# Optimization experiments

Measured on AMD Instinct MI355X. Metric: run time of the kernel, lower is better.

The kernel has to match this reference:

```python
import jax, jax.numpy as jnp
import numpy as np

B, L = 1024, 1024
NCAT, NNUM = 20, 10
CAT_BUCKETS, SEQ_VOCAB = 100000, 50000
E, A, H, QH = 32, 128, 256, 256
TOPK = 30


def _init(key, shape, scale=0.02):
    return scale * jax.random.normal(key, shape, dtype=jnp.float32)


def setup_inputs() -> dict:
    key = jax.random.key(0)
    ks = jax.random.split(key, 24)
    z = lambda *s: jnp.zeros(s, dtype=jnp.float32)
    return {
        "cats": jax.random.randint(ks[0], (B, NCAT), 0, CAT_BUCKETS + 1),
        "nums": jax.random.normal(ks[1], (B, NNUM), dtype=jnp.float32),
        "seqs": jax.random.randint(ks[2], (B, L), 0, SEQ_VOCAB + 1),
        "tgt_ids": jax.random.randint(ks[3], (B,), 0, CAT_BUCKETS + 1),
        "cat_emb": _init(ks[4], (CAT_BUCKETS + 1, E)),
        "seq_emb": _init(ks[5], (SEQ_VOCAB + 1, E)),
        "Wnum": _init(ks[6], (NNUM, E)), "bnum": z(E),
        "Wq": _init(ks[7], (E, A)), "Wk": _init(ks[8], (E, A)), "Wv": _init(ks[9], (E, A)),
        "Wo": _init(ks[10], (A, E)), "bo": z(E),
        "Wpool": _init(ks[11], (NCAT * E, E)), "bpool": z(E),
        "Wmlp": _init(ks[12], (4 * E, H)), "bmlp": z(H),
        "q1_W1": _init(ks[13], (H, QH)), "q1_b1": z(QH),
        "q1_W2": _init(ks[14], (H, QH)), "q1_b2": z(QH),
        "q1_Wp": _init(ks[15], (QH, H)), "q1_bp": z(H),
        "q2_W1": _init(ks[16], (H, QH)), "q2_b1": z(QH),
        "q2_W2": _init(ks[17], (H, QH)), "q2_b2": z(QH),
        "q2_Wp": _init(ks[18], (QH, H)), "q2_bp": z(H),
        "Wout": _init(ks[19], (H, 1)), "bout": z(1),
    }


def _qnn(x, W1, b1, W2, b2, Wp, bp):
    # Quadratic neural block (QIN-style): Hadamard product of two linear maps,
    # projected back with a residual connection. Dropout is identity in eval.
    quad = (x @ W1 + b1) * (x @ W2 + b2)
    return x + quad @ Wp + bp


def reference(cats, nums, seqs, tgt_ids, cat_emb, seq_emb, Wnum, bnum, Wq, Wk, Wv,
              Wo, bo, Wpool, bpool, Wmlp, bmlp,
              q1_W1, q1_b1, q1_W2, q1_b2, q1_Wp, q1_bp,
              q2_W1, q2_b1, q2_W2, q2_b2, q2_Wp, q2_bp, Wout, bout):
    cat_e = cat_emb[cats]                                   # [B, NCAT, E]
    cat_pool = cat_e.reshape(cat_e.shape[0], -1) @ Wpool + bpool   # [B, E]
    num_e = nums @ Wnum + bnum                              # [B, E]
    tgt_e = cat_emb[tgt_ids]                                # [B, E] (tgt_emb shares cat_emb)
    seq_e = seq_emb[seqs]                                   # [B, L, E]

    q = tgt_e @ Wq                                          # [B, A]
    k = seq_e @ Wk                                          # [B, L, A]
    v = seq_e @ Wv                                          # [B, L, A]
    scores = jnp.einsum('ba,bla->bl', q, k) / jnp.sqrt(jnp.float32(A))

    # top-k + scatter mask + masked softmax == softmax over the top-k scores,
    # scattered implicitly via gather of the selected values.
    vals, idx = jax.lax.top_k(scores, TOPK)                 # [B, TOPK]
    w = jax.nn.softmax(vals, axis=1)                        # [B, TOPK]
    v_sel = jnp.take_along_axis(v, idx[:, :, None], axis=1)  # [B, TOPK, A]
    interest = jnp.einsum('bk,bka->ba', w, v_sel) @ Wo + bo  # [B, E]

    fused = jnp.concatenate([tgt_e, interest, cat_pool, num_e], axis=1)  # [B, 4E]
    h = jax.nn.relu(fused @ Wmlp + bmlp)                    # [B, H], dropout=eval
    h = _qnn(h, q1_W1, q1_b1, q1_W2, q1_b2, q1_Wp, q1_bp)
    h = _qnn(h, q2_W1, q2_b1, q2_W2, q2_b2, q2_Wp, q2_bp)
    return (h @ Wout + bout)[:, 0]                          # [B]
```

## Files before the change

kernel.cpp:

```cpp
#include <hip/hip_runtime.h>
#include <hip/hip_fp16.h>

#define B_ 1024
#define L_ 1024
#define NCAT_ 20
#define NNUM_ 10
#define E_ 32
#define A_ 128
#define H_ 256
#define TOPK_ 30
#define INV_SQRT_A 0.08838834764831845f

__device__ __forceinline__ void fma4(float4& a, float s, const float4 w) {
    a.x += s * w.x; a.y += s * w.y; a.z += s * w.z; a.w += s * w.w;
}
__device__ __forceinline__ float4 ldh4(const __half* p) {
    float2 rw = *(const float2*)p;
    const __half2* h = (const __half2*)&rw;
    float2 a = __half22float2(h[0]);
    float2 b = __half22float2(h[1]);
    return make_float4(a.x, a.y, b.x, b.y);
}
__device__ __forceinline__ void ldh24(const __half2* p, float4& w1, float4& w2) {
    float4 rw = *(const float4*)p;
    const __half2* h = (const __half2*)&rw;
    float2 f0 = __half22float2(h[0]), f1 = __half22float2(h[1]);
    float2 f2 = __half22float2(h[2]), f3 = __half22float2(h[3]);
    w1 = make_float4(f0.x, f1.x, f2.x, f3.x);
    w2 = make_float4(f0.y, f1.y, f2.y, f3.y);
}
__device__ __forceinline__ unsigned sortable(float f) {
    unsigned u = __float_as_uint(f);
    return (u & 0x80000000u) ? ~u : (u | 0x80000000u);
}
__device__ __forceinline__ float unsortable(unsigned s) {
    unsigned u = (s & 0x80000000u) ? (s ^ 0x80000000u) : ~s;
    return __uint_as_float(u);
}

#define K1_GRID 1356
__global__ __launch_bounds__(256) void fused_prep_kernel(
    const int* __restrict__ cats, const float* __restrict__ nums,
    const int* __restrict__ tgt_ids, const float* __restrict__ cat_emb,
    const float* __restrict__ Wnum, const float* __restrict__ bnum,
    const float* __restrict__ Wq, const float* __restrict__ Wk,
    const float* __restrict__ Wv, const float* __restrict__ Wo,
    const float* __restrict__ Wpool, const float* __restrict__ bpool,
    const float* __restrict__ seq_emb, const float* __restrict__ Wmlp,
    const float* __restrict__ q1W1, const float* __restrict__ q1W2,
    const float* __restrict__ q2W1, const float* __restrict__ q2W2,
    const float* __restrict__ q1Wp, const float* __restrict__ q2Wp,
    float* __restrict__ p_out, float* __restrict__ fused, float* __restrict__ M,
    __half2* __restrict__ seq_h2, __half2* __restrict__ Wmlp_h2,
    __half2* __restrict__ W12_1, __half2* __restrict__ W12_2,
    __half2* __restrict__ Wp1_h2, __half2* __restrict__ Wp2_h2)
{
    const int blk = blockIdx.x;
    const int t = threadIdx.x;

    if (blk < 256) {
        __shared__ float ce[4][NCAT_ * E_];
        __shared__ float tg[4][E_];
        __shared__ float nm[4][NNUM_];
        __shared__ float qs[4][A_];
        __shared__ float part[8][4][E_];
        const int r0 = blk * 4;

        for (int idx = t; idx < 640; idx += 256) {
            const int q = idx >> 3, f4 = idx & 7;
            const int row = q / 20, cat = q % 20;
            const int tok = cats[(r0 + row) * NCAT_ + cat];
            ((float4*)&ce[row][cat * 32])[f4] =
                ((const float4*)(cat_emb + (size_t)tok * 32))[f4];
        }
        if (t < 32) {
            const int row = t >> 3, f4 = t & 7;
            const int tok = tgt_ids[r0 + row];
            ((float4*)&tg[row][0])[f4] =
                ((const float4*)(cat_emb + (size_t)tok * 32))[f4];
        }
        if (t >= 64 && t < 104) {
            const int x = t - 64;
            nm[x / 10][x % 10] = nums[(r0 + x / 10) * NNUM_ + x % 10];
        }
        __syncthreads();

        {
            const int w = t >> 6, lane = t & 63;
            float q0 = 0.f, q1 = 0.f;
#pragma unroll
            for (int e = 0; e < E_; ++e) {
                float te = tg[w][e];
                q0 += te * Wq[e * A_ + lane];
                q1 += te * Wq[e * A_ + lane + 64];
            }
            qs[w][lane] = q0; qs[w][lane + 64] = q1;
        }

        {
            const int iseg = t >> 5;
            const int row = (t >> 3) & 3;
            const int c0 = (t & 7) * 4;
            float4 acc = make_float4(0.f, 0.f, 0.f, 0.f);
            const int i0 = iseg * 80;
            for (int i = i0; i < i0 + 80; ++i) {
                float4 wv = *(const float4*)(Wpool + i * 32 + c0);
                fma4(acc, ce[row][i], wv);
            }
            *(float4*)&part[iseg][row][c0] = acc;
        }
        __syncthreads();

        if (t < 128) {
            const int row = t >> 5, c = t & 31;
            const int b = r0 + row;
            float s = bpool[c];
#pragma unroll
            for (int g = 0; g < 8; ++g) s += part[g][row][c];
            fused[b * 128 + 64 + c] = s;
            fused[b * 128 + c] = tg[row][c];

            float ne = bnum[c];
#pragma unroll
            for (int n = 0; n < NNUM_; ++n) ne += nm[row][n] * Wnum[n * 32 + c];
            fused[b * 128 + 96 + c] = ne;

            float pv = 0.f;
#pragma unroll 8
            for (int a = 0; a < A_; ++a) pv += Wk[c * A_ + a] * qs[row][a];
            p_out[b * 32 + c] = pv;
        }
        return;
    }

    if (blk < 1280) {
        int x = (blk - 256) * 256 + t;
        for (; x < 800016; x += 1024 * 256) {
            float2 v = ((const float2*)seq_emb)[x];
            seq_h2[x] = __float22half2_rn(v);
        }
        return;
    }

    if (blk < 1284) {
        const int o = (blk - 1280) * 256 + t;
        const int j = o >> 5, e = o & 31;
        float sm = 0.f;
#pragma unroll 8
        for (int a = 0; a < A_; ++a) sm += Wv[j * A_ + a] * Wo[a * E_ + e];
        M[o] = sm;
        return;
    }

    if (blk < 1348) {
        int x = (blk - 1284) * 256 + t;
        for (; x < 65536; x += 64 * 256) {
            W12_1[x] = __float22half2_rn(make_float2(q1W1[x], q1W2[x]));
            W12_2[x] = __float22half2_rn(make_float2(q2W1[x], q2W2[x]));
        }
        return;
    }

    {
        int x = (blk - 1348) * 256 + t;
        for (; x < 16384; x += 8 * 256)
            Wmlp_h2[x] = __float22half2_rn(((const float2*)Wmlp)[x]);
        x = (blk - 1348) * 256 + t;
        for (; x < 32768; x += 8 * 256) {
            Wp1_h2[x] = __float22half2_rn(((const float2*)q1Wp)[x]);
            Wp2_h2[x] = __float22half2_rn(((const float2*)q2Wp)[x]);
        }
    }
}

#define RM 4
__global__ __launch_bounds__(512) void score_mlp_kernel(
    const int* __restrict__ seqs, const __half* __restrict__ seq_h,
    const float* __restrict__ seq_emb, const float* __restrict__ p,
    const float* __restrict__ M, const float* __restrict__ bo,
    const float* __restrict__ fused,
    const __half* __restrict__ Wmlp_h, const float* __restrict__ bmlp,
    const __half2* __restrict__ W12_1, const float* __restrict__ b11,
    const float* __restrict__ b12, const __half* __restrict__ Wp1_h,
    const float* __restrict__ b1p,
    const __half2* __restrict__ W12_2, const float* __restrict__ b21,
    const float* __restrict__ b22, const __half* __restrict__ Wp2_h,
    const float* __restrict__ b2p,
    const float* __restrict__ Wout, const float* __restrict__ bout,
    float* __restrict__ out)
{
    const int b0 = blockIdx.x * RM;
    const int tid = threadIdx.x;

    __shared__ float sc[RM][L_];
    __shared__ float ps[RM][E_];
    __shared__ float sw[RM][32];
    __shared__ int   stok[RM][32];
    __shared__ float xs[RM][128];
    __shared__ float hs[RM][H_];
    __shared__ float ts[RM][H_];
    __shared__ float part[8][RM][H_];
    __shared__ float red[8];

    if (tid < 128) ps[tid >> 5][tid & 31] = p[(b0 + (tid >> 5)) * 32 + (tid & 31)];
    __syncthreads();

    {
        const int row = tid >> 7;
        const int s = tid & 127;
        const int bb = b0 + row;
#pragma unroll
        for (int jj = 0; jj < 4; ++jj) {
            const int l1 = jj * 256 + s;
            const int l2 = l1 + 128;
            const int tok1 = seqs[bb * L_ + l1];
            const int tok2 = seqs[bb * L_ + l2];
            float4 buf[2][4];
            const float4* r1 = (const float4*)(seq_h + (size_t)tok1 * 32);
            const float4* r2 = (const float4*)(seq_h + (size_t)tok2 * 32);
#pragma unroll
            for (int i = 0; i < 4; ++i) buf[0][i] = r1[i];
#pragma unroll
            for (int i = 0; i < 4; ++i) buf[1][i] = r2[i];

            float acc0 = 0.f, acc1 = 0.f;
#pragma unroll
            for (int i = 0; i < 4; ++i) {
                const __half2* h1 = (const __half2*)&buf[0][i];
                const __half2* h2 = (const __half2*)&buf[1][i];
#pragma unroll
                for (int u = 0; u < 4; ++u) {
                    float2 f1 = __half22float2(h1[u]);
                    float2 f2 = __half22float2(h2[u]);
                    acc0 += f1.x * ps[row][i * 8 + 2 * u] + f1.y * ps[row][i * 8 + 2 * u + 1];
                    acc1 += f2.x * ps[row][i * 8 + 2 * u] + f2.y * ps[row][i * 8 + 2 * u + 1];
                }
            }
            sc[row][l1] = acc0 * INV_SQRT_A;
            sc[row][l2] = acc1 * INV_SQRT_A;
        }
    }
    if (tid < 384) {
        const int r = tid / 96, c0 = tid % 96;
        const int c = (c0 < 32) ? c0 : (c0 + 32);
        xs[r][c] = fused[(b0 + r) * 128 + c];
    }
    __syncthreads();

    if (tid < 256) {
        const int w = tid >> 6;
        const int lane = tid & 63;
        const int bb = b0 + w;

        unsigned long long key[16];
#pragma unroll
        for (int j = 0; j < 16; ++j) {
            const int l = j * 64 + lane;
            key[j] = ((unsigned long long)sortable(sc[w][l]) << 10)
                   | (unsigned)(1023 - l);
        }
#pragma unroll
        for (int a = 0; a < 15; ++a)
#pragma unroll
            for (int j = 0; j < 15 - a; ++j) {
                const bool swp = key[j] < key[j + 1];
                const unsigned long long hi = swp ? key[j + 1] : key[j];
                const unsigned long long lo = swp ? key[j] : key[j + 1];
                key[j] = hi; key[j + 1] = lo;
            }

        float myv = -1e30f; int myl = 0;
        unsigned long long front = key[0];
        for (int k = 0; k < TOPK_; ++k) {
            unsigned long long wk = front;
#pragma unroll
            for (int off = 32; off > 0; off >>= 1) {
                unsigned long long o = __shfl_xor(wk, off);
                if (o > wk) wk = o;
            }
            if (lane == k) {
                myv = unsortable((unsigned)(wk >> 10));
                myl = 1023 - (int)(wk & 1023);
            }
            if (front == wk) {
#pragma unroll
                for (int j = 0; j < 15; ++j) key[j] = key[j + 1];
                key[15] = 0ULL;
                front = key[0];
            }
        }

        float m = myv;
#pragma unroll
        for (int off = 32; off > 0; off >>= 1) m = fmaxf(m, __shfl_xor(m, off));
        float e = (lane < TOPK_) ? expf(myv - m) : 0.f;
        float s = e;
#pragma unroll
        for (int off = 32; off > 0; off >>= 1) s += __shfl_xor(s, off);
        if (lane < TOPK_) {
            sw[w][lane]   = e / s;
            stok[w][lane] = seqs[bb * L_ + myl];
        }

        if (lane < E_) {
            float acc = 0.f;
#pragma unroll
            for (int k = 0; k < TOPK_; ++k)
                acc += sw[w][k] * seq_emb[(size_t)stok[w][k] * 32 + lane];
            sc[w][lane] = acc;
        }
        if (lane < E_) {
            float acc = bo[lane];
#pragma unroll
            for (int j = 0; j < E_; ++j) acc += sc[w][j] * M[j * E_ + lane];
            xs[w][32 + lane] = acc;
        }
    }
    __syncthreads();

    const int cg = tid & 63;
    const int iseg = tid >> 6;
    const int c0 = cg * 4;

    {
        float4 acc[RM];
#pragma unroll
        for (int r = 0; r < RM; ++r) acc[r] = make_float4(0.f, 0.f, 0.f, 0.f);
        const int i0 = iseg * 16;
#pragma unroll
        for (int iq = 0; iq < 4; ++iq) {
            const int i = i0 + iq * 4;
            float4 w[4], xv[RM];
#pragma unroll
            for (int u = 0; u < 4; ++u) w[u] = ldh4(Wmlp_h + (i + u) * H_ + c0);
#pragma unroll
            for (int r = 0; r < RM; ++r) xv[r] = *(const float4*)(&xs[r][i]);
#pragma unroll
            for (int r = 0; r < RM; ++r) {
                fma4(acc[r], xv[r].x, w[0]); fma4(acc[r], xv[r].y, w[1]);
                fma4(acc[r], xv[r].z, w[2]); fma4(acc[r], xv[r].w, w[3]);
            }
        }
#pragma unroll
        for (int r = 0; r < RM; ++r) *(float4*)&part[iseg][r][c0] = acc[r];
    }
    __syncthreads();
    for (int o = tid; o < RM * H_; o += 512) {
        const int r = o >> 8, c = o & 255;
        float s = bmlp[c];
#pragma unroll
        for (int sg = 0; sg < 8; ++sg) s += part[sg][r][c];
        hs[r][c] = fmaxf(s, 0.f);
    }
    __syncthreads();

    const __half2* W12s[2] = { W12_1, W12_2 };
    const float* b1s[2] = { b11, b21 }; const float* b2s[2] = { b12, b22 };
    const __half* Wps[2] = { Wp1_h, Wp2_h }; const float* bps[2] = { b1p, b2p };

    for (int q = 0; q < 2; ++q) {
        const __half2* __restrict__ W12 = W12s[q];
        const __half*  __restrict__ Wp  = Wps[q];
        float4 a1[RM], a2[RM];
        {
#pragma unroll
            for (int r = 0; r < RM; ++r) {
                a1[r] = make_float4(0.f, 0.f, 0.f, 0.f);
                a2[r] = make_float4(0.f, 0.f, 0.f, 0.f);
            }
            const int i0 = iseg * 32;
#pragma unroll 2
            for (int iq = 0; iq < 8; ++iq) {
                const int i = i0 + iq * 4;
                float4 w1[4], w2[4], hv[RM];
#pragma unroll
                for (int u = 0; u < 4; ++u) ldh24(W12 + (i + u) * H_ + c0, w1[u], w2[u]);
#pragma unroll
                for (int r = 0; r < RM; ++r) hv[r] = *(const float4*)(&hs[r][i]);
#pragma unroll
                for (int r = 0; r < RM; ++r) {
                    fma4(a1[r], hv[r].x, w1[0]); fma4(a1[r], hv[r].y, w1[1]);
                    fma4(a1[r], hv[r].z, w1[2]); fma4(a1[r], hv[r].w, w1[3]);
                    fma4(a2[r], hv[r].x, w2[0]); fma4(a2[r], hv[r].y, w2[1]);
                    fma4(a2[r], hv[r].z, w2[2]); fma4(a2[r], hv[r].w, w2[3]);
                }
            }
        }
#pragma unroll
        for (int r = 0; r < RM; ++r) *(float4*)&part[iseg][r][c0] = a1[r];
        __syncthreads();
        {
            const float* b1 = b1s[q];
            for (int o = tid; o < RM * H_; o += 512) {
                const int r = o >> 8, c = o & 255;
                float t1 = b1[c];
#pragma unroll
                for (int sg = 0; sg < 8; ++sg) t1 += part[sg][r][c];
                ts[r][c] = t1;
            }
        }
        __syncthreads();
#pragma unroll
        for (int r = 0; r < RM; ++r) *(float4*)&part[iseg][r][c0] = a2[r];
        __syncthreads();
        {
            const float* b2 = b2s[q];
            for (int o = tid; o < RM * H_; o += 512) {
                const int r = o >> 8, c = o & 255;
                float t2 = b2[c];
#pragma unroll
                for (int sg = 0; sg < 8; ++sg) t2 += part[sg][r][c];
                ts[r][c] = ts[r][c] * t2;
            }
        }
        __syncthreads();

        {
            float4 ap[RM];
#pragma unroll
            for (int r = 0; r < RM; ++r) ap[r] = make_float4(0.f, 0.f, 0.f, 0.f);
            const int i0 = iseg * 32;
#pragma unroll 2
            for (int iq = 0; iq < 8; ++iq) {
                const int i = i0 + iq * 4;
                float4 w[4], tv[RM];
#pragma unroll
                for (int u = 0; u < 4; ++u) w[u] = ldh4(Wp + (i + u) * H_ + c0);
#pragma unroll
                for (int r = 0; r < RM; ++r) tv[r] = *(const float4*)(&ts[r][i]);
#pragma unroll
                for (int r = 0; r < RM; ++r) {
                    fma4(ap[r], tv[r].x, w[0]); fma4(ap[r], tv[r].y, w[1]);
                    fma4(ap[r], tv[r].z, w[2]); fma4(ap[r], tv[r].w, w[3]);
                }
            }
#pragma unroll
            for (int r = 0; r < RM; ++r) *(float4*)&part[iseg][r][c0] = ap[r];
        }
        __syncthreads();
        {
            const float* bp = bps[q];
            for (int o = tid; o < RM * H_; o += 512) {
                const int r = o >> 8, c = o & 255;
                float s = bp[c];
#pragma unroll
                for (int sg = 0; sg < 8; ++sg) s += part[sg][r][c];
                hs[r][c] += s;
            }
        }
        __syncthreads();
    }

    {
        const int r = tid >> 7, jj = tid & 127;
        float sum = hs[r][jj] * Wout[jj] + hs[r][jj + 128] * Wout[jj + 128];
#pragma unroll
        for (int off = 32; off > 0; off >>= 1) sum += __shfl_down(sum, off);
        if ((tid & 63) == 0) red[tid >> 6] = sum;
        __syncthreads();
        if (tid < RM) out[b0 + tid] = red[2 * tid] + red[2 * tid + 1] + bout[0];
    }
}

extern "C" void kernel_launch(void* const* d_in, const int* in_sizes, int n_in,
                              void* d_out, int out_size, void* d_ws, size_t ws_size,
                              hipStream_t stream) {
    const int*   cats    = (const int*)d_in[0];
    const float* nums    = (const float*)d_in[1];
    const int*   seqs    = (const int*)d_in[2];
    const int*   tgt_ids = (const int*)d_in[3];
    const float* cat_emb = (const float*)d_in[4];
    const float* seq_emb = (const float*)d_in[5];
    const float* Wnum    = (const float*)d_in[6];
    const float* bnum    = (const float*)d_in[7];
    const float* Wq      = (const float*)d_in[8];
    const float* Wk      = (const float*)d_in[9];
    const float* Wv      = (const float*)d_in[10];
    const float* Wo      = (const float*)d_in[11];
    const float* bo      = (const float*)d_in[12];
    const float* Wpool   = (const float*)d_in[13];
    const float* bpool   = (const float*)d_in[14];
    const float* Wmlp    = (const float*)d_in[15];
    const float* bmlp    = (const float*)d_in[16];
    const float* q1_W1   = (const float*)d_in[17];
    const float* q1_b1   = (const float*)d_in[18];
    const float* q1_W2   = (const float*)d_in[19];
    const float* q1_b2   = (const float*)d_in[20];
    const float* q1_Wp   = (const float*)d_in[21];
    const float* q1_bp   = (const float*)d_in[22];
    const float* q2_W1   = (const float*)d_in[23];
    const float* q2_b1   = (const float*)d_in[24];
    const float* q2_W2   = (const float*)d_in[25];
    const float* q2_b2   = (const float*)d_in[26];
    const float* q2_Wp   = (const float*)d_in[27];
    const float* q2_bp   = (const float*)d_in[28];
    const float* Wout    = (const float*)d_in[29];
    const float* bout    = (const float*)d_in[30];

    float* ws = (float*)d_ws;
    float*   p       = ws;
    float*   fused   = ws + 32768;
    float*   M       = ws + 163840;
    __half2* seq_h2  = (__half2*)(ws + 164864);
    __half2* Wmlp_h2 = (__half2*)(ws + 964928);
    __half2* W12_1   = (__half2*)(ws + 981312);
    __half2* W12_2   = (__half2*)(ws + 1046848);
    __half2* Wp1_h2  = (__half2*)(ws + 1112384);
    __half2* Wp2_h2  = (__half2*)(ws + 1145152);

    float* out = (float*)d_out;

    fused_prep_kernel<<<K1_GRID, 256, 0, stream>>>(
        cats, nums, tgt_ids, cat_emb, Wnum, bnum, Wq, Wk, Wv, Wo,
        Wpool, bpool, seq_emb, Wmlp,
        q1_W1, q1_W2, q2_W1, q2_W2, q1_Wp, q2_Wp,
        p, fused, M, seq_h2, Wmlp_h2, W12_1, W12_2, Wp1_h2, Wp2_h2);

    score_mlp_kernel<<<B_ / RM, 512, 0, stream>>>(
        seqs, (const __half*)seq_h2, seq_emb, p, M, bo, fused,
        (const __half*)Wmlp_h2, bmlp,
        W12_1, q1_b1, q1_b2, (const __half*)Wp1_h2, q1_bp,
        W12_2, q2_b1, q2_b2, (const __half*)Wp2_h2, q2_bp,
        Wout, bout, out);
}
```

Before: 181.5 us.

## Halve rows per block and merge QNN partial reductions into one pass

Each block now processes 2 batch rows instead of 4, so twice as many blocks are launched, and launch bounds request 4 blocks per CU for more occupancy. The two quadratic-branch partial sums are written to separate shared buffers and reduced together, which removes two barriers and a second store/reduce pass per QNN layer. The per-thread reductions are simplified to a single output element per thread. Each block still loads the full MLP weights, so weight traffic per output row doubles, and shared memory grows with the extra partial buffer.

```diff
diff --git a/kernel.cpp b/kernel.cpp
--- a/kernel.cpp
+++ b/kernel.cpp
@@ -173,8 +173,8 @@
     }
 }
 
-#define RM 4
-__global__ __launch_bounds__(512) void score_mlp_kernel(
+#define RM 2
+__global__ __launch_bounds__(512, 4) void score_mlp_kernel(
     const int* __restrict__ seqs, const __half* __restrict__ seq_h,
     const float* __restrict__ seq_emb, const float* __restrict__ p,
     const float* __restrict__ M, const float* __restrict__ bo,
@@ -199,20 +199,22 @@
     __shared__ float xs[RM][128];
     __shared__ float hs[RM][H_];
     __shared__ float ts[RM][H_];
-    __shared__ float part[8][RM][H_];
+    __shared__ float partA[8][RM][H_];
+    __shared__ float partB[8][RM][H_];
     __shared__ float red[8];
 
-    if (tid < 128) ps[tid >> 5][tid & 31] = p[(b0 + (tid >> 5)) * 32 + (tid & 31)];
+    if (tid < RM * 32)
+        ps[tid >> 5][tid & 31] = p[(b0 + (tid >> 5)) * 32 + (tid & 31)];
     __syncthreads();
 
     {
-        const int row = tid >> 7;
-        const int s = tid & 127;
+        const int row = tid >> 8;
+        const int s = tid & 255;
         const int bb = b0 + row;
 #pragma unroll
-        for (int jj = 0; jj < 4; ++jj) {
-            const int l1 = jj * 256 + s;
-            const int l2 = l1 + 128;
+        for (int jj = 0; jj < 2; ++jj) {
+            const int l1 = jj * 512 + s;
+            const int l2 = l1 + 256;
             const int tok1 = seqs[bb * L_ + l1];
             const int tok2 = seqs[bb * L_ + l2];
             float4 buf[2][4];
@@ -240,14 +242,14 @@
             sc[row][l2] = acc1 * INV_SQRT_A;
         }
     }
-    if (tid < 384) {
+    if (tid < RM * 96) {
         const int r = tid / 96, c0 = tid % 96;
         const int c = (c0 < 32) ? c0 : (c0 + 32);
         xs[r][c] = fused[(b0 + r) * 128 + c];
     }
     __syncthreads();
 
-    if (tid < 256) {
+    if (tid < RM * 64) {
         const int w = tid >> 6;
         const int lane = tid & 63;
         const int bb = b0 + w;
@@ -321,6 +323,8 @@
     const int cg = tid & 63;
     const int iseg = tid >> 6;
     const int c0 = cg * 4;
+    const int rr = tid >> 8;
+    const int rc = tid & 255;
 
     {
         float4 acc[RM];
@@ -342,15 +346,14 @@
             }
         }
 #pragma unroll
-        for (int r = 0; r < RM; ++r) *(float4*)&part[iseg][r][c0] = acc[r];
+        for (int r = 0; r < RM; ++r) *(float4*)&partA[iseg][r][c0] = acc[r];
     }
     __syncthreads();
-    for (int o = tid; o < RM * H_; o += 512) {
-        const int r = o >> 8, c = o & 255;
-        float s = bmlp[c];
-#pragma unroll
-        for (int sg = 0; sg < 8; ++sg) s += part[sg][r][c];
-        hs[r][c] = fmaxf(s, 0.f);
+    {
+        float s = bmlp[rc];
+#pragma unroll
+        for (int sg = 0; sg < 8; ++sg) s += partA[sg][rr][rc];
+        hs[rr][rc] = fmaxf(s, 0.f);
     }
     __syncthreads();
 
@@ -361,8 +364,8 @@
     for (int q = 0; q < 2; ++q) {
         const __half2* __restrict__ W12 = W12s[q];
         const __half*  __restrict__ Wp  = Wps[q];
-        float4 a1[RM], a2[RM];
         {
+            float4 a1[RM], a2[RM];
 #pragma unroll
             for (int r = 0; r < RM; ++r) {
                 a1[r] = make_float4(0.f, 0.f, 0.f, 0.f);
@@ -385,33 +388,21 @@
                     fma4(a2[r], hv[r].z, w2[2]); fma4(a2[r], hv[r].w, w2[3]);
                 }
             }
-        }
-#pragma unroll
-        for (int r = 0; r < RM; ++r) *(float4*)&part[iseg][r][c0] = a1[r];
+#pragma unroll
+            for (int r = 0; r < RM; ++r) {
+                *(float4*)&partA[iseg][r][c0] = a1[r];
+                *(float4*)&partB[iseg][r][c0] = a2[r];
+            }
+        }
         __syncthreads();
         {
-            const float* b1 = b1s[q];
-            for (int o = tid; o < RM * H_; o += 512) {
-                const int r = o >> 8, c = o & 255;
-                float t1 = b1[c];
-#pragma unroll
-                for (int sg = 0; sg < 8; ++sg) t1 += part[sg][r][c];
-                ts[r][c] = t1;
-            }
-        }
-        __syncthreads();
-#pragma unroll
-        for (int r = 0; r < RM; ++r) *(float4*)&part[iseg][r][c0] = a2[r];
-        __syncthreads();
-        {
-            const float* b2 = b2s[q];
-            for (int o = tid; o < RM * H_; o += 512) {
-                const int r = o >> 8, c = o & 255;
-                float t2 = b2[c];
-#pragma unroll
-                for (int sg = 0; sg < 8; ++sg) t2 += part[sg][r][c];
-                ts[r][c] = ts[r][c] * t2;
-            }
+            float t1 = b1s[q][rc], t2 = b2s[q][rc];
+#pragma unroll
+            for (int sg = 0; sg < 8; ++sg) {
+                t1 += partA[sg][rr][rc];
+                t2 += partB[sg][rr][rc];
+            }
+            ts[rr][rc] = t1 * t2;
         }
         __syncthreads();
 
@@ -435,28 +426,27 @@
                 }
             }
 #pragma unroll
-            for (int r = 0; r < RM; ++r) *(float4*)&part[iseg][r][c0] = ap[r];
+            for (int r = 0; r < RM; ++r) *(float4*)&partA[iseg][r][c0] = ap[r];
         }
         __syncthreads();
         {
-            const float* bp = bps[q];
-            for (int o = tid; o < RM * H_; o += 512) {
-                const int r = o >> 8, c = o & 255;
-                float s = bp[c];
-#pragma unroll
-                for (int sg = 0; sg < 8; ++sg) s += part[sg][r][c];
-                hs[r][c] += s;
-            }
+            float s = bps[q][rc];
+#pragma unroll
+            for (int sg = 0; sg < 8; ++sg) s += partA[sg][rr][rc];
+            hs[rr][rc] += s;
         }
         __syncthreads();
     }
 
     {
-        const int r = tid >> 7, jj = tid & 127;
-        float sum = hs[r][jj] * Wout[jj] + hs[r][jj + 128] * Wout[jj + 128];
+        const int r = (tid >> 7) & (RM - 1);
+        const int jj = tid & 127;
+        float sum = 0.f;
+        if (tid < RM * 128)
+            sum = hs[r][jj] * Wout[jj] + hs[r][jj + 128] * Wout[jj + 128];
 #pragma unroll
         for (int off = 32; off > 0; off >>= 1) sum += __shfl_down(sum, off);
-        if ((tid & 63) == 0) red[tid >> 6] = sum;
+        if (tid < RM * 128 && (tid & 63) == 0) red[tid >> 6] = sum;
         __syncthreads();
         if (tid < RM) out[b0 + tid] = red[2 * tid] + red[2 * tid + 1] + bout[0];
     }
```

Result: slower. 185.4 us (+2.1%).
